# Kernel tuning notes

Measured on AMD Instinct MI355X. Metric: run time of the kernel, lower is better.

Reference implementation:

```python
import jax, jax.numpy as jnp
import numpy as np

B, C, H, W, D = 4, 64, 64, 64, 4
CQ = C // 8  # query/key channels


def setup_inputs() -> dict:
    key = jax.random.key(0)
    ks = jax.random.split(key, 10)
    x2d = jax.random.normal(ks[0], (B, C, H, W, D), dtype=jnp.float32)
    x3d = jax.random.normal(ks[1], (B, C, H, W, D), dtype=jnp.float32)
    # 1x1 Conv3d weights collapsed to (out_ch, in_ch) matrices + biases
    Wq = jax.random.normal(ks[2], (CQ, C), dtype=jnp.float32) * 0.05
    bq = jax.random.normal(ks[3], (CQ,), dtype=jnp.float32) * 0.05
    Wk = jax.random.normal(ks[4], (CQ, C), dtype=jnp.float32) * 0.05
    bk = jax.random.normal(ks[5], (CQ,), dtype=jnp.float32) * 0.05
    Wv = jax.random.normal(ks[6], (C, C), dtype=jnp.float32) * 0.05
    bv = jax.random.normal(ks[7], (C,), dtype=jnp.float32) * 0.05
    gamma = jax.random.normal(ks[8], (1,), dtype=jnp.float32)
    return {"x2d": x2d, "x3d": x3d, "Wq": Wq, "bq": bq, "Wk": Wk,
            "bk": bk, "Wv": Wv, "bv": bv, "gamma": gamma}


def _conv1x1(Wmat, bias, x):
    # x: (B, C, D, H, W); 1x1x1 Conv3d == channel matmul
    y = jnp.einsum('oc,bcdhw->bodhw', Wmat, x)
    return y + bias[None, :, None, None, None]


def reference(x2d, x3d, Wq, bq, Wk, bk, Wv, bv, gamma):
    x = jnp.transpose(x2d, (0, 1, 4, 2, 3))  # (B, C, D, H, W)
    b, c, d, h, w = x.shape
    n = h * w
    q = _conv1x1(Wq, bq, x).reshape(b, -1, n)   # (B, CQ*D, N)
    k = _conv1x1(Wk, bk, x).reshape(b, -1, n)   # (B, CQ*D, N)
    v = _conv1x1(Wv, bv, x).reshape(b, -1, n)   # (B, C*D, N)
    energy = jnp.einsum('bkn,bkm->bnm', q, k)   # (B, N, N), no scaling (faithful)
    attn = jax.nn.softmax(energy, axis=-1)
    # out[b,c,i] = sum_j attn[b,i,j] * v[b,c,j]
    out = jnp.einsum('bcm,bnm->bcn', v, attn)
    out = out.reshape(b, c, d, h, w)
    out = jnp.transpose(out, (0, 1, 3, 4, 2))   # back to (B, C, H, W, D)
    return gamma * out + x3d
```

## Files before the change

kernel.cpp:

```cpp
#include <hip/hip_runtime.h>
#include <hip/hip_bf16.h>

#define CH 64
#define NN 4096
#define SS 16384

typedef __attribute__((ext_vector_type(8))) short bf16x8;
typedef __attribute__((ext_vector_type(4))) float f32x4;

#define QB_OFF 0
#define KB_OFF 524288
#define VT_OFF 1048576

static __device__ __forceinline__ float fexp2(float x) {
    float r;
    asm("v_exp_f32 %0, %1" : "=v"(r) : "v"(x));
    return r;
}

static __device__ __forceinline__ uint cvtpk(float a, float b) {
    uint r;
    asm("v_cvt_pk_bf16_f32 %0, %1, %2" : "=v"(r) : "v"(a), "v"(b));
    return r;
}

static __device__ __forceinline__ void gld_lds16(const ushort* g, ushort* l) {
    __builtin_amdgcn_global_load_lds(
        (const __attribute__((address_space(1))) void*)g,
        (__attribute__((address_space(3))) void*)l, 16, 0, 0);
}

__global__ __launch_bounds__(256) void qkv_kernel(
    const float* __restrict__ x,
    const float* __restrict__ Wq, const float* __restrict__ bq,
    const float* __restrict__ Wk, const float* __restrict__ bk,
    const float* __restrict__ Wv, const float* __restrict__ bv,
    ushort* __restrict__ qb, ushort* __restrict__ kb, ushort* __restrict__ vt)
{
    __shared__ __align__(16) ushort Tqk[128 * 40];
    __shared__ __align__(16) ushort Tv[80 * 144];

    const int blk = blockIdx.x;
    const int xcd = blk & 7, jb = blk >> 3;
    const int b = xcd >> 1;
    const int sup = ((xcd & 1) << 4) | (jb & 15);
    const int og = jb >> 4;
    const int tid = threadIdx.x;
    const int nl = tid >> 2, d = tid & 3;

    const int vcnt = (og < 2) ? 12 : 20;
    const int vo0 = (og == 0) ? 0 : (og == 1) ? 12 : (og == 2) ? 24 : 44;

    const float qscale = (og == 0) ? 1.4426950408889634f : 1.0f;

    const float* xb = x + (size_t)b * CH * SS + sup * 512;

    for (int t = 0; t < 2; ++t) {
        const float* xp = xb + t * 256 + tid;
        float xr[CH];
#pragma unroll
        for (int c = 0; c < CH; ++c) xr[c] = xp[(size_t)c * SS];

        const int slot = 32 * (nl >> 4) + 8 * ((nl >> 2) & 3) + 4 * t + (nl & 3);

        if (og < 2) {
            const float* Wqk = (og == 0) ? Wq : Wk;
            const float* bqk = (og == 0) ? bq : bk;
            ushort* trow = &Tqk[(t * 64 + nl) * 40 + d];
#pragma unroll
            for (int o = 0; o < 8; o += 2) {
                float a0 = bqk[o], a1 = bqk[o + 1];
#pragma unroll
                for (int c = 0; c < CH; ++c) {
                    a0 = fmaf(Wqk[o * CH + c],       xr[c], a0);
                    a1 = fmaf(Wqk[(o + 1) * CH + c], xr[c], a1);
                }
                uint wp = cvtpk(a0 * qscale, a1 * qscale);
                trow[o * 4]       = (ushort)wp;
                trow[(o + 1) * 4] = (ushort)(wp >> 16);
            }
        }
        ushort* vcol = &Tv[d * 144 + slot];
        const float* Wvb = Wv + vo0 * CH;
        const float* bvb = bv + vo0;
        if (og < 2) {
#pragma unroll
            for (int j = 0; j < 12; j += 2) {
                float a0 = bvb[j], a1 = bvb[j + 1];
#pragma unroll
                for (int c = 0; c < CH; ++c) {
                    a0 = fmaf(Wvb[j * CH + c],       xr[c], a0);
                    a1 = fmaf(Wvb[(j + 1) * CH + c], xr[c], a1);
                }
                uint wp = cvtpk(a0, a1);
                vcol[(j * 4) * 144]       = (ushort)wp;
                vcol[((j + 1) * 4) * 144] = (ushort)(wp >> 16);
            }
        } else {
#pragma unroll
            for (int j = 0; j < 20; j += 2) {
                float a0 = bvb[j], a1 = bvb[j + 1];
#pragma unroll
                for (int c = 0; c < CH; ++c) {
                    a0 = fmaf(Wvb[j * CH + c],       xr[c], a0);
                    a1 = fmaf(Wvb[(j + 1) * CH + c], xr[c], a1);
                }
                uint wp = cvtpk(a0, a1);
                vcol[(j * 4) * 144]       = (ushort)wp;
                vcol[((j + 1) * 4) * 144] = (ushort)(wp >> 16);
            }
        }
    }
    __syncthreads();

    if (og < 2) {
        ushort* dst = (og == 0 ? qb : kb);
#pragma unroll
        for (int jj = 0; jj < 2; ++jj) {
            int idx = jj * 256 + tid;
            int row = idx >> 2, seg = idx & 3;
            *(uint4*)(dst + ((size_t)(b * NN + sup * 128 + row)) * 32 + seg * 8)
                = *(const uint4*)&Tqk[row * 40 + seg * 8];
        }
    }
    const int nchunks = vcnt * 64;
    ushort* vout = vt + ((size_t)((b * 32 + sup) * 256 + vo0 * 4)) * 144;
#pragma unroll
    for (int j = 0; j < 5; ++j) {
        int idx = j * 256 + tid;
        if (idx < nchunks) {
            int row = idx >> 4, seg = idx & 15;
            *(uint4*)(vout + (size_t)row * 144 + seg * 8)
                = *(const uint4*)&Tv[row * 144 + seg * 8];
        }
    }
}

__global__ __launch_bounds__(256, 2) void flash_kernel(
    const ushort* __restrict__ qb, const ushort* __restrict__ kb,
    const ushort* __restrict__ vt, const float* __restrict__ x3d,
    const float* __restrict__ gptr, float* __restrict__ out)
{
    __shared__ __align__(16) ushort Vls[2][128 * 144];
    __shared__ float lbuf[4 * 4 * 16];

    const int tid = threadIdx.x;
    const int xcd = blockIdx.x & 7, jb = blockIdx.x >> 3;
    const int b   = xcd >> 1;
    const int r0  = (jb & 63) << 6;
    const int cvh = xcd & 1;
    const int w = tid >> 6, lane = tid & 63, q = lane >> 4, l15 = lane & 15;

    bf16x8 Qf[4];
#pragma unroll
    for (int rt = 0; rt < 4; ++rt)
        Qf[rt] = *(const bf16x8*)(qb + (size_t)(b * NN + r0 + 16 * rt + l15) * 32 + 8 * q);

    f32x4 acc[8][4];
#pragma unroll
    for (int i = 0; i < 8; ++i)
#pragma unroll
        for (int j = 0; j < 4; ++j) acc[i][j] = (f32x4){0.f, 0.f, 0.f, 0.f};
    float l_acc[4] = {0.f, 0.f, 0.f, 0.f};

    const ushort* kgl = kb + (size_t)b * NN * 32 + (16 * w + l15) * 32 + 8 * q;

    const ushort* vgl = vt + ((size_t)(b * 32) * 256 + 128 * cvh) * 144;

#pragma unroll
    for (int i = 0; i < 9; ++i)
        gld_lds16(vgl + (size_t)(i * 256 + tid) * 8,
                  (ushort*)Vls[0] + (i * 256 + tid) * 8);

    bf16x8 Kc0 = *(const bf16x8*)(kgl);
    bf16x8 Kc1 = *(const bf16x8*)(kgl + 2048);
    bf16x8 Ka0 = *(const bf16x8*)(kgl + 2 * 2048);
    bf16x8 Ka1 = *(const bf16x8*)(kgl + 3 * 2048);
    bf16x8 Kn0, Kn1;

    f32x4 S0[4], S1[4];
    __builtin_amdgcn_s_setprio(1);
#pragma unroll
    for (int rt = 0; rt < 4; ++rt)
        S0[rt] = __builtin_amdgcn_mfma_f32_16x16x32_bf16(
            Kc0, Qf[rt], (f32x4){0.f, 0.f, 0.f, 0.f}, 0, 0, 0);
#pragma unroll
    for (int rt = 0; rt < 4; ++rt)
        S1[rt] = __builtin_amdgcn_mfma_f32_16x16x32_bf16(
            Kc1, Qf[rt], (f32x4){0.f, 0.f, 0.f, 0.f}, 0, 0, 0);
    __builtin_amdgcn_s_setprio(0);

    for (int pt = 0; pt < 32; ++pt) {
        __syncthreads();
        if (pt < 31) {
            const ushort* src = vgl + (size_t)(pt + 1) * 36864;
            ushort* dst = (ushort*)Vls[(pt + 1) & 1];
#pragma unroll
            for (int i = 0; i < 9; ++i)
                gld_lds16(src + (size_t)(i * 256 + tid) * 8, dst + (i * 256 + tid) * 8);
        }
        if (pt < 30) {
            Kn0 = *(const bf16x8*)(kgl + (size_t)(2 * pt + 4) * 2048);
            Kn1 = *(const bf16x8*)(kgl + (size_t)(2 * pt + 5) * 2048);
        }

        bf16x8 Pb[4];
#pragma unroll
        for (int rt = 0; rt < 4; ++rt) {
            float e0 = fexp2(S0[rt][0]), e1 = fexp2(S0[rt][1]);
            float e2 = fexp2(S0[rt][2]), e3 = fexp2(S0[rt][3]);
            float f0 = fexp2(S1[rt][0]), f1 = fexp2(S1[rt][1]);
            float f2 = fexp2(S1[rt][2]), f3 = fexp2(S1[rt][3]);
            l_acc[rt] += ((e0 + e1) + (e2 + e3)) + ((f0 + f1) + (f2 + f3));
            union { uint u[4]; bf16x8 v; } pk;
            pk.u[0] = cvtpk(e0, e1);
            pk.u[1] = cvtpk(e2, e3);
            pk.u[2] = cvtpk(f0, f1);
            pk.u[3] = cvtpk(f2, f3);
            Pb[rt] = pk.v;
        }

        if (pt < 31) {
            __builtin_amdgcn_s_setprio(1);
#pragma unroll
            for (int rt = 0; rt < 4; ++rt)
                S0[rt] = __builtin_amdgcn_mfma_f32_16x16x32_bf16(
                    Ka0, Qf[rt], (f32x4){0.f, 0.f, 0.f, 0.f}, 0, 0, 0);
#pragma unroll
            for (int rt = 0; rt < 4; ++rt)
                S1[rt] = __builtin_amdgcn_mfma_f32_16x16x32_bf16(
                    Ka1, Qf[rt], (f32x4){0.f, 0.f, 0.f, 0.f}, 0, 0, 0);
            __builtin_amdgcn_s_setprio(0);
            Ka0 = Kn0; Ka1 = Kn1;
        }

        const ushort* vb = Vls[pt & 1] + 32 * w + 8 * q;
        __builtin_amdgcn_s_setprio(1);
#pragma unroll
        for (int cvt = 0; cvt < 8; ++cvt) {
            bf16x8 Va = *(const bf16x8*)(vb + (16 * cvt + l15) * 144);
#pragma unroll
            for (int rt = 0; rt < 4; ++rt)
                acc[cvt][rt] = __builtin_amdgcn_mfma_f32_16x16x32_bf16(
                    Va, Pb[rt], acc[cvt][rt], 0, 0, 0);
        }
        __builtin_amdgcn_s_setprio(0);
    }

#pragma unroll
    for (int rt = 0; rt < 4; ++rt) {
        float v = l_acc[rt];
        v += __shfl_xor(v, 16);
        v += __shfl_xor(v, 32);
        if (lane < 16) lbuf[(w * 4 + rt) * 16 + lane] = v;
    }
    __syncthreads();
    const float linv = 1.f / (lbuf[(0 + w) * 16 + l15] + lbuf[(4 + w) * 16 + l15] +
                              lbuf[(8 + w) * 16 + l15] + lbuf[(12 + w) * 16 + l15]);
    const float gl = gptr[0] * linv;

    f32x4* Obuf = (f32x4*)&Vls[0][0];
#pragma unroll
    for (int cvt = 0; cvt < 8; ++cvt) {
        __syncthreads();
#pragma unroll
        for (int rt = 0; rt < 4; ++rt)
            Obuf[(w * 64 + lane) * 5 + rt] = acc[cvt][rt];
        __syncthreads();
        f32x4 o = Obuf[lane * 5 + w];
        o += Obuf[(64 + lane) * 5 + w];
        o += Obuf[(128 + lane) * 5 + w];
        o += Obuf[(192 + lane) * 5 + w];
        size_t addr = ((size_t)(b * CH + 32 * cvh + 4 * cvt + q) * NN
                       + (r0 + 16 * w + l15)) * 4;
        float4 xr = *(const float4*)(x3d + addr);
        float4 res;
        res.x = fmaf(gl, o[0], xr.x);
        res.y = fmaf(gl, o[1], xr.y);
        res.z = fmaf(gl, o[2], xr.z);
        res.w = fmaf(gl, o[3], xr.w);
        *(float4*)(out + addr) = res;
    }
}

extern "C" void kernel_launch(void* const* d_in, const int* in_sizes, int n_in,
                              void* d_out, int out_size, void* d_ws, size_t ws_size,
                              hipStream_t stream)
{
    const float* x2d = (const float*)d_in[0];
    const float* x3d = (const float*)d_in[1];
    const float* Wq  = (const float*)d_in[2];
    const float* bq  = (const float*)d_in[3];
    const float* Wk  = (const float*)d_in[4];
    const float* bk  = (const float*)d_in[5];
    const float* Wv  = (const float*)d_in[6];
    const float* bv  = (const float*)d_in[7];
    const float* gma = (const float*)d_in[8];

    ushort* wsb = (ushort*)d_ws;

    qkv_kernel<<<512, 256, 0, stream>>>(x2d, Wq, bq, Wk, bk, Wv, bv,
                                        wsb + QB_OFF, wsb + KB_OFF, wsb + VT_OFF);
    flash_kernel<<<512, 256, 0, stream>>>(wsb + QB_OFF, wsb + KB_OFF, wsb + VT_OFF,
                                          x3d, gma, (float*)d_out);
}
```

Baseline: 156.4 us.

## Compute QKV projection with bf16 MFMA instead of scalar FMA loops

Replaces the per-thread scalar fp32 FMA projection in the QKV kernel with bf16 MFMA 16x16x32 tiles. Weights (with log2e folded into Q) and an x tile are staged in LDS, then each wave computes all 80 output rows for its spatial columns. The block work split changes from output-channel groups to spatial chunks, so each block reads a distinct x slice rather than several blocks re-reading the same one. The input and weights now pass through bf16 before the projection, which lowers projection precision. Outputs are written with scattered 2-byte global stores instead of coalesced 16-byte stores from LDS.

```diff
diff --git a/kernel.cpp b/kernel.cpp
--- a/kernel.cpp
+++ b/kernel.cpp
@@ -4,6 +4,7 @@
 #define CH 64
 #define NN 4096
 #define SS 16384
+#define LOG2E 1.4426950408889634f
 
 typedef __attribute__((ext_vector_type(8))) short bf16x8;
 typedef __attribute__((ext_vector_type(4))) float f32x4;
@@ -37,101 +38,99 @@
     const float* __restrict__ Wv, const float* __restrict__ bv,
     ushort* __restrict__ qb, ushort* __restrict__ kb, ushort* __restrict__ vt)
 {
-    __shared__ __align__(16) ushort Tqk[128 * 40];
-    __shared__ __align__(16) ushort Tv[80 * 144];
+    __shared__ __align__(16) ushort Wl[80 * 72];
+    __shared__ __align__(16) ushort Xl[128 * 72];
+    __shared__ __align__(16) float  Bl[80];
 
     const int blk = blockIdx.x;
     const int xcd = blk & 7, jb = blk >> 3;
     const int b = xcd >> 1;
     const int sup = ((xcd & 1) << 4) | (jb & 15);
-    const int og = jb >> 4;
+    const int sch = jb >> 4;
     const int tid = threadIdx.x;
-    const int nl = tid >> 2, d = tid & 3;
-
-    const int vcnt = (og < 2) ? 12 : 20;
-    const int vo0 = (og == 0) ? 0 : (og == 1) ? 12 : (og == 2) ? 24 : 44;
-
-    const float qscale = (og == 0) ? 1.4426950408889634f : 1.0f;
-
-    const float* xb = x + (size_t)b * CH * SS + sup * 512;
-
-    for (int t = 0; t < 2; ++t) {
-        const float* xp = xb + t * 256 + tid;
-        float xr[CH];
-#pragma unroll
-        for (int c = 0; c < CH; ++c) xr[c] = xp[(size_t)c * SS];
-
+
+#pragma unroll
+    for (int r = 0; r < 2; ++r) {
+        int idx = r * 256 + tid, m = idx >> 6, c = idx & 63;
+        Wl[m * 72 + c] = (ushort)(cvtpk(Wq[m * 64 + c] * LOG2E, 0.f) & 0xffff);
+    }
+#pragma unroll
+    for (int r = 0; r < 2; ++r) {
+        int idx = r * 256 + tid, m = idx >> 6, c = idx & 63;
+        Wl[(8 + m) * 72 + c] = (ushort)(cvtpk(Wk[m * 64 + c], 0.f) & 0xffff);
+    }
+#pragma unroll
+    for (int r = 0; r < 16; ++r) {
+        int idx = r * 256 + tid, m = idx >> 6, c = idx & 63;
+        Wl[(16 + m) * 72 + c] = (ushort)(cvtpk(Wv[m * 64 + c], 0.f) & 0xffff);
+    }
+    if (tid < 80)
+        Bl[tid] = (tid < 8) ? bq[tid] * LOG2E
+                : (tid < 16) ? bk[tid - 8] : bv[tid - 16];
+
+    const int slot32 = tid & 31, cb = tid >> 5;
+    const int s0 = sup * 512 + sch * 128;
+    const float* xb = x + (size_t)(b * 64 + cb * 8) * SS + s0 + 4 * slot32;
+    uint ru[4][4];
+#pragma unroll
+    for (int j = 0; j < 4; ++j) {
+        float4 fA = *(const float4*)(xb + (2 * j) * SS);
+        float4 fB = *(const float4*)(xb + (2 * j + 1) * SS);
+        ru[0][j] = cvtpk(fA.x, fB.x);
+        ru[1][j] = cvtpk(fA.y, fB.y);
+        ru[2][j] = cvtpk(fA.z, fB.z);
+        ru[3][j] = cvtpk(fA.w, fB.w);
+    }
+#pragma unroll
+    for (int v = 0; v < 4; ++v) {
+        uint4 pk = make_uint4(ru[0][0], ru[0][1], ru[0][2], ru[0][3]);
+        pk = make_uint4(ru[v][0], ru[v][1], ru[v][2], ru[v][3]);
+        *(uint4*)&Xl[(4 * slot32 + v) * 72 + cb * 8] = pk;
+    }
+    __syncthreads();
+
+    const int w = tid >> 6, lane = tid & 63, q = lane >> 4, l15 = lane & 15;
+#pragma unroll
+    for (int i = 0; i < 2; ++i) {
+        const int nt = 2 * w + i;
+        bf16x8 b0 = *(const bf16x8*)&Xl[(nt * 16 + l15) * 72 + 8 * q];
+        bf16x8 b1 = *(const bf16x8*)&Xl[(nt * 16 + l15) * 72 + 8 * q + 32];
+
+        const int s_loc = nt * 16 + l15;
+        const int dd = l15 & 3;
+        const int nsup = sch * 32 + nt * 4 + (l15 >> 2);
+        const int t = nsup >> 6, nl = nsup & 63;
         const int slot = 32 * (nl >> 4) + 8 * ((nl >> 2) & 3) + 4 * t + (nl & 3);
-
-        if (og < 2) {
-            const float* Wqk = (og == 0) ? Wq : Wk;
-            const float* bqk = (og == 0) ? bq : bk;
-            ushort* trow = &Tqk[(t * 64 + nl) * 40 + d];
-#pragma unroll
-            for (int o = 0; o < 8; o += 2) {
-                float a0 = bqk[o], a1 = bqk[o + 1];
-#pragma unroll
-                for (int c = 0; c < CH; ++c) {
-                    a0 = fmaf(Wqk[o * CH + c],       xr[c], a0);
-                    a1 = fmaf(Wqk[(o + 1) * CH + c], xr[c], a1);
-                }
-                uint wp = cvtpk(a0 * qscale, a1 * qscale);
-                trow[o * 4]       = (ushort)wp;
-                trow[(o + 1) * 4] = (ushort)(wp >> 16);
+        const int n = sup * 128 + nsup;
+        (void)s_loc;
+
+#pragma unroll
+        for (int mt = 0; mt < 5; ++mt) {
+            bf16x8 a0 = *(const bf16x8*)&Wl[(mt * 16 + l15) * 72 + 8 * q];
+            bf16x8 a1 = *(const bf16x8*)&Wl[(mt * 16 + l15) * 72 + 8 * q + 32];
+            f32x4 acc = __builtin_amdgcn_mfma_f32_16x16x32_bf16(
+                a0, b0, (f32x4){0.f, 0.f, 0.f, 0.f}, 0, 0, 0);
+            acc = __builtin_amdgcn_mfma_f32_16x16x32_bf16(a1, b1, acc, 0, 0, 0);
+            f32x4 bias = *(const f32x4*)&Bl[mt * 16 + 4 * q];
+            acc += bias;
+            uint u01 = cvtpk(acc[0], acc[1]);
+            uint u23 = cvtpk(acc[2], acc[3]);
+            if (mt == 0) {
+                ushort* dst = (q < 2)
+                    ? qb + ((size_t)(b * NN + n)) * 32 + 16 * q + dd
+                    : kb + ((size_t)(b * NN + n)) * 32 + 16 * (q - 2) + dd;
+                dst[0]  = (ushort)u01;
+                dst[4]  = (ushort)(u01 >> 16);
+                dst[8]  = (ushort)u23;
+                dst[12] = (ushort)(u23 >> 16);
+            } else {
+                ushort* dst = vt + ((size_t)((b * 32 + sup) * 256
+                              + ((mt - 1) * 16 + 4 * q) * 4 + dd)) * 144 + slot;
+                dst[0 * 576] = (ushort)u01;
+                dst[1 * 576] = (ushort)(u01 >> 16);
+                dst[2 * 576] = (ushort)u23;
+                dst[3 * 576] = (ushort)(u23 >> 16);
             }
-        }
-        ushort* vcol = &Tv[d * 144 + slot];
-        const float* Wvb = Wv + vo0 * CH;
-        const float* bvb = bv + vo0;
-        if (og < 2) {
-#pragma unroll
-            for (int j = 0; j < 12; j += 2) {
-                float a0 = bvb[j], a1 = bvb[j + 1];
-#pragma unroll
-                for (int c = 0; c < CH; ++c) {
-                    a0 = fmaf(Wvb[j * CH + c],       xr[c], a0);
-                    a1 = fmaf(Wvb[(j + 1) * CH + c], xr[c], a1);
-                }
-                uint wp = cvtpk(a0, a1);
-                vcol[(j * 4) * 144]       = (ushort)wp;
-                vcol[((j + 1) * 4) * 144] = (ushort)(wp >> 16);
-            }
-        } else {
-#pragma unroll
-            for (int j = 0; j < 20; j += 2) {
-                float a0 = bvb[j], a1 = bvb[j + 1];
-#pragma unroll
-                for (int c = 0; c < CH; ++c) {
-                    a0 = fmaf(Wvb[j * CH + c],       xr[c], a0);
-                    a1 = fmaf(Wvb[(j + 1) * CH + c], xr[c], a1);
-                }
-                uint wp = cvtpk(a0, a1);
-                vcol[(j * 4) * 144]       = (ushort)wp;
-                vcol[((j + 1) * 4) * 144] = (ushort)(wp >> 16);
-            }
-        }
-    }
-    __syncthreads();
-
-    if (og < 2) {
-        ushort* dst = (og == 0 ? qb : kb);
-#pragma unroll
-        for (int jj = 0; jj < 2; ++jj) {
-            int idx = jj * 256 + tid;
-            int row = idx >> 2, seg = idx & 3;
-            *(uint4*)(dst + ((size_t)(b * NN + sup * 128 + row)) * 32 + seg * 8)
-                = *(const uint4*)&Tqk[row * 40 + seg * 8];
-        }
-    }
-    const int nchunks = vcnt * 64;
-    ushort* vout = vt + ((size_t)((b * 32 + sup) * 256 + vo0 * 4)) * 144;
-#pragma unroll
-    for (int j = 0; j < 5; ++j) {
-        int idx = j * 256 + tid;
-        if (idx < nchunks) {
-            int row = idx >> 4, seg = idx & 15;
-            *(uint4*)(vout + (size_t)row * 144 + seg * 8)
-                = *(const uint4*)&Tv[row * 144 + seg * 8];
         }
     }
 }
```

Result: faster. 143.1 us (-8.5%).
